# Kernel tuning notes

Hardware: AMD Instinct MI355X
Metric: run time of the kernel (lower is better)

The kernel has to match this reference:

```python
import jax, jax.numpy as jnp
import numpy as np

EPS = 1e-6
TEMP_GEO = 0.07
W_LOCAL = 0.5
W_SHARP = 0.5


def _l2norm(x):
    return x / jnp.clip(jnp.linalg.norm(x, axis=-1, keepdims=True), 1e-12)


def setup_inputs() -> dict:
    key = jax.random.key(0)
    ks = jax.random.split(key, 6)
    B, L, S, C = 8, 1024, 1024, 128
    N, P = 8, 256
    q_geo = _l2norm(jax.random.normal(ks[0], (B, L, C), jnp.float32))
    geo_pos = _l2norm(jax.random.normal(ks[1], (B, S, C), jnp.float32))
    label = jax.random.randint(ks[2], (B, L, S), 0, 2, jnp.int32)
    q_cl = jax.random.normal(ks[3], (N, P, C), jnp.float32)
    cl_pos = jax.random.normal(ks[4], (N, P, C), jnp.float32)
    idx = jax.random.randint(ks[5], (N,), 0, P, jnp.int32)
    return {"q_geo": q_geo, "q_cl": q_cl, "geo_pos": geo_pos,
            "cl_pos": cl_pos, "label": label, "idx": idx}


def _masked_mean(v, m):
    # per-sample mean over the [L,S] plane of entries where m is True
    m = m.astype(v.dtype)
    return jnp.sum(v * m, axis=(1, 2)) / jnp.maximum(jnp.sum(m, axis=(1, 2)), 1.0)


def _loftr_loss(conf, label):
    # standard LoFTR coarse CE loss (LoFTRLoss source absent from repo snippet)
    conf = jnp.clip(conf, EPS, 1.0 - EPS)
    pos = label == 1
    neg = label == 0
    pos_loss = _masked_mean(-jnp.log(conf), pos)          # [B]
    neg_loss = _masked_mean(-jnp.log(1.0 - conf), neg)    # [B]
    loss = pos_loss + neg_loss
    return jnp.mean(loss), jnp.mean(pos_loss), jnp.mean(neg_loss)


def _geometric_loss(q, k, label):
    sim = jnp.einsum('blc,bsc->bls', q, k) / TEMP_GEO        # [B,L,S]
    conf = jax.nn.softmax(sim, axis=1) * jax.nn.softmax(sim, axis=2)
    return _loftr_loss(conf, label)


def _sharpness_loss(q, k, label):
    sim = (1.0 + jnp.einsum('blc,bsc->bls', q, k)) / 2.0     # [B,L,S]
    # column stats (over L, dim=0 per sample) -> sharpness1 [B,S]
    s1 = (jnp.max(sim, axis=1) - jnp.mean(sim, axis=1)) / jnp.std(sim, axis=1, ddof=1)
    sharp1 = jax.nn.softmax(s1, axis=-1)
    # row stats (over S, dim=1 per sample) -> sharpness2 [B,L]
    s2 = (jnp.max(sim, axis=2) - jnp.mean(sim, axis=2)) / jnp.std(sim, axis=2, ddof=1)
    sharp2 = jax.nn.softmax(s2, axis=-1)
    simc = jnp.clip(sim, EPS, 1.0 - EPS)
    nll = -jnp.log(simc)
    pos = (label == 1).astype(simc.dtype)
    neg = (label == 0)
    loss1 = jnp.sum(nll * sharp1[:, None, :] * pos, axis=(1, 2))   # [B]
    loss2 = jnp.sum(nll * sharp2[:, :, None] * pos, axis=(1, 2))   # [B]
    loss3 = _masked_mean(-jnp.log(1.0 - simc), neg)                # [B]
    losses = (loss1 + loss2) / 2.0 + loss3
    return sharp1, jnp.mean(losses)


def _contrast_loss(q, all_k):
    # intended math of GeCoContrast: full cosine matrix, diag positives, tail negatives
    N = q.shape[0]
    sim = (1.0 + _l2norm(q) @ _l2norm(all_k).T) / 2.0   # [N, M]
    sim = jnp.clip(sim, EPS, 1.0 - EPS)
    l_pos = jnp.diagonal(sim[:, :N])                    # [N]
    l_neg = sim[:, N:]                                  # [N, M-N]
    return (jnp.mean(-jnp.log(l_pos)) + jnp.mean(-jnp.log(1.0 - l_neg))) / 2.0


def _forward(q_geo, q_cl, geo_pos, cl_pos, label, idx):
    loss_geo, geo_pos_loss, geo_neg_loss = _geometric_loss(q_geo, geo_pos, label)
    sharpness, loss_sharp = _sharpness_loss(q_geo, geo_pos, label)
    loss_geo = ((1.0 - W_SHARP) * loss_geo + W_SHARP * loss_sharp) * W_LOCAL

    N, P, C = q_cl.shape
    ar = jnp.arange(N)
    q_sel = q_cl[ar, idx]                               # [N,C]
    sel = cl_pos[ar, idx]                               # [N,C] positives moved to slot 0
    first = cl_pos[:, 0, :]
    swapped = cl_pos.at[ar, idx].set(first).at[:, 0, :].set(sel)
    cl_pos_save = sel
    all_k = jnp.concatenate([swapped[:, 0, :],
                             swapped[:, 1:, :].reshape(N * (P - 1), C)], axis=0)
    loss_cl = _contrast_loss(q_sel, all_k) * (1.0 - W_LOCAL)

    total = loss_geo + loss_cl
    return (sharpness, cl_pos_save, total, geo_pos_loss, geo_neg_loss, loss_sharp, loss_cl)


def reference(q_geo, q_cl, geo_pos, cl_pos, label, idx):
    return _forward(q_geo, q_cl, geo_pos, cl_pos, label, idx)
```

## Files before the change

kernel.cpp:

```cpp
#include <hip/hip_runtime.h>
#include <math.h>

#define BB 8
#define LL 1024
#define SS 1024
#define CC 128
#define NN 8
#define PP 256

static constexpr float EPS       = 1e-6f;
static constexpr float ONE_M_EPS = 1.0f - 1e-6f;
static constexpr float INV_T     = 1.0f / 0.07f;
static constexpr float NLL_MAX   = 13.815511f;
static constexpr float NLL_MIN   = 1.0000005e-6f;

static constexpr size_t DOTSZ      = (size_t)BB * LL * SS;
static constexpr size_t OFF_LSER   = DOTSZ;
static constexpr size_t OFF_LSEC   = DOTSZ + 16384;
static constexpr size_t OFF_SHARP2 = DOTSZ + 32768;
static constexpr size_t OFF_RP     = DOTSZ + 40960;
static constexpr size_t OFF_CP     = OFF_RP + 524288;
static constexpr size_t OFF_ACC    = OFF_CP + 524288;
static constexpr size_t OFF_ACCCL  = OFF_ACC + 48;
static constexpr size_t OFF_QN     = OFF_ACC + 64;

static constexpr int OUT_CLSAVE = 8192;
static constexpr int OUT_SCAL   = 9216;

typedef __bf16 bf16x8 __attribute__((ext_vector_type(8)));
typedef float  floatx4 __attribute__((ext_vector_type(4)));

__device__ __forceinline__ bf16x8 mkfrag(unsigned a, unsigned b, unsigned c, unsigned d) {
    uint4 t = make_uint4(a, b, c, d);
    return __builtin_bit_cast(bf16x8, t);
}

__device__ __forceinline__ void split_f4(float4 x,
                                         unsigned& hp0, unsigned& hp1,
                                         unsigned& lp0, unsigned& lp1) {
    unsigned u0 = __builtin_bit_cast(unsigned, x.x);
    unsigned u1 = __builtin_bit_cast(unsigned, x.y);
    unsigned u2 = __builtin_bit_cast(unsigned, x.z);
    unsigned u3 = __builtin_bit_cast(unsigned, x.w);
    unsigned r0 = u0 + 0x7FFFu + ((u0 >> 16) & 1u);
    unsigned r1 = u1 + 0x7FFFu + ((u1 >> 16) & 1u);
    unsigned r2 = u2 + 0x7FFFu + ((u2 >> 16) & 1u);
    unsigned r3 = u3 + 0x7FFFu + ((u3 >> 16) & 1u);
    float s0 = x.x - __builtin_bit_cast(float, r0 & 0xFFFF0000u);
    float s1 = x.y - __builtin_bit_cast(float, r1 & 0xFFFF0000u);
    float s2 = x.z - __builtin_bit_cast(float, r2 & 0xFFFF0000u);
    float s3 = x.w - __builtin_bit_cast(float, r3 & 0xFFFF0000u);
    hp0 = __builtin_amdgcn_perm(r1, r0, 0x07060302u);
    hp1 = __builtin_amdgcn_perm(r3, r2, 0x07060302u);
    lp0 = __builtin_amdgcn_perm(__builtin_bit_cast(unsigned, s1),
                                __builtin_bit_cast(unsigned, s0), 0x07060302u);
    lp1 = __builtin_amdgcn_perm(__builtin_bit_cast(unsigned, s3),
                                __builtin_bit_cast(unsigned, s2), 0x07060302u);
}

__device__ __forceinline__ void frag_from_lds(const float* tile, int row, int q,
                                              bf16x8& hi, bf16x8& lo) {
    const float* rp = tile + row * 32;
    int sw = row & 7;
    float4 x0 = *(const float4*)(rp + (((q * 2)     ^ sw) * 4));
    float4 x1 = *(const float4*)(rp + (((q * 2 + 1) ^ sw) * 4));
    unsigned h0, h1, h2, h3, l0, l1, l2, l3;
    split_f4(x0, h0, h1, l0, l1);
    split_f4(x1, h2, h3, l2, l3);
    hi = mkfrag(h0, h1, h2, h3);
    lo = mkfrag(l0, l1, l2, l3);
}

__global__ __launch_bounds__(256, 2) void gemm_dot(const float* __restrict__ A,
                                                   const float* __restrict__ Bm,
                                                   const float* __restrict__ q_cl,
                                                   const float* __restrict__ cl_pos,
                                                   const int* __restrict__ idx,
                                                   float* __restrict__ out,
                                                   float* __restrict__ dot,
                                                   float* __restrict__ ws) {
    __shared__ __align__(16) float ldsA[2][128 * 32];
    __shared__ __align__(16) float ldsB[2][128 * 32];

    int tid  = threadIdx.x;
    int lane = tid & 63;
    int w    = tid >> 6;

    if (blockIdx.x == 512) {
        if (tid < 52) ws[OFF_ACC + tid] = 0.0f;
        for (int n = w; n < NN; n += 4) {
            int in = idx[n];
            const float* q = q_cl + ((size_t)(n * PP + in)) * CC;
            float2 qv = *(const float2*)(q + 2 * lane);
            float ss = qv.x * qv.x + qv.y * qv.y;
            for (int o = 32; o; o >>= 1) ss += __shfl_xor(ss, o);
            float inv = 1.0f / fmaxf(sqrtf(ss), 1e-12f);
            *(float2*)(ws + OFF_QN + n * 128 + 2 * lane) = make_float2(qv.x * inv, qv.y * inv);
            const float* cp = cl_pos + ((size_t)(n * PP + in)) * CC;
            float2 cv = *(const float2*)(cp + 2 * lane);
            *(float2*)(out + OUT_CLSAVE + n * 128 + 2 * lane) = cv;
        }
        return;
    }

    int t  = blockIdx.x;
    int b  = t >> 6;
    int rm = t & 63;
    int bl = rm >> 3, bs = rm & 7;
    int R0 = bl * 128, C0 = bs * 128;

    const float* Ab = A  + ((size_t)b * LL + R0) * CC;
    const float* Bb = Bm + ((size_t)b * SS + C0) * CC;

    const float* src  = (w >= 2) ? Bb : Ab;
    float* dst0 = (w >= 2) ? ldsB[0] : ldsA[0];
    float* dst1 = (w >= 2) ? ldsB[1] : ldsA[1];
    int L       = ((w & 1) << 6) | lane;
    int rowoff  = L >> 3;
    int chunk   = L & 7;
    int swz4    = (chunk ^ (rowoff & 7)) * 4;

    int fl   = lane & 15;
    int quad = lane >> 4;
    int wr   = w >> 1, wc = w & 1;
    int Rw   = wr * 64, Cw = wc * 64;

    floatx4 acc[4][4];
#pragma unroll
    for (int i = 0; i < 4; i++)
#pragma unroll
        for (int j = 0; j < 4; j++) acc[i][j] = (floatx4){0.f, 0.f, 0.f, 0.f};

    float4 rg[8];
#pragma unroll
    for (int i = 0; i < 8; i++)
        rg[i] = *(const float4*)(src + (size_t)(i * 16 + rowoff) * CC + chunk * 4);
#pragma unroll
    for (int i = 0; i < 8; i++)
        *(float4*)(dst0 + (i * 16 + rowoff) * 32 + swz4) = rg[i];
    __syncthreads();

    for (int ks = 0; ks < 4; ks++) {
        const float* la = (ks & 1) ? ldsA[1] : ldsA[0];
        const float* lb = (ks & 1) ? ldsB[1] : ldsB[0];
        float* nxt = ((ks + 1) & 1) ? dst1 : dst0;
        if (ks < 3) {
            int k0 = (ks + 1) * 32;
#pragma unroll
            for (int i = 0; i < 8; i++)
                rg[i] = *(const float4*)(src + (size_t)(i * 16 + rowoff) * CC + k0 + chunk * 4);
        }
        bf16x8 ah[4], al[4];
#pragma unroll
        for (int mt = 0; mt < 4; mt++)
            frag_from_lds(la, Rw + mt * 16 + fl, quad, ah[mt], al[mt]);
#pragma unroll
        for (int nt = 0; nt < 4; nt++) {
            bf16x8 bh, blo;
            frag_from_lds(lb, Cw + nt * 16 + fl, quad, bh, blo);
#pragma unroll
            for (int mt = 0; mt < 4; mt++) {
                acc[mt][nt] = __builtin_amdgcn_mfma_f32_16x16x32_bf16(ah[mt], bh,  acc[mt][nt], 0, 0, 0);
                acc[mt][nt] = __builtin_amdgcn_mfma_f32_16x16x32_bf16(ah[mt], blo, acc[mt][nt], 0, 0, 0);
                acc[mt][nt] = __builtin_amdgcn_mfma_f32_16x16x32_bf16(al[mt], bh,  acc[mt][nt], 0, 0, 0);
            }
        }
        if (ks < 3) {
#pragma unroll
            for (int i = 0; i < 8; i++)
                *(float4*)(nxt + (i * 16 + rowoff) * 32 + swz4) = rg[i];
        }
        __syncthreads();
    }

#pragma unroll
    for (int mt = 0; mt < 4; mt++)
#pragma unroll
        for (int nt = 0; nt < 4; nt++) {
            int col = C0 + Cw + nt * 16 + fl;
#pragma unroll
            for (int r = 0; r < 4; r++) {
                int row = R0 + Rw + mt * 16 + quad * 4 + r;
                dot[((size_t)(b * 1024 + row)) * 1024 + col] = acc[mt][nt][r];
            }
        }

    int stile = bs * 2 + wc;
    int ltile = bl * 2 + wr;
    float ces[4], cmx[4], csm[4], csq[4];
#pragma unroll
    for (int nt = 0; nt < 4; nt++) { ces[nt] = 0.f; cmx[nt] = -1e30f; csm[nt] = 0.f; csq[nt] = 0.f; }
#pragma unroll
    for (int mt = 0; mt < 4; mt++) {
#pragma unroll
        for (int r = 0; r < 4; r++) {
            float es = 0.f, mx = -1e30f, sm = 0.f, sq = 0.f;
#pragma unroll
            for (int nt = 0; nt < 4; nt++) {
                float d  = acc[mt][nt][r];
                float e  = __expf(d * INV_T);
                float s2 = fmaf(0.5f, d, 0.5f);
                es += e; mx = fmaxf(mx, s2); sm += s2; sq += s2 * s2;
                ces[nt] += e; cmx[nt] = fmaxf(cmx[nt], s2); csm[nt] += s2; csq[nt] += s2 * s2;
            }
            for (int o = 1; o < 16; o <<= 1) {
                es += __shfl_xor(es, o);
                mx = fmaxf(mx, __shfl_xor(mx, o));
                sm += __shfl_xor(sm, o);
                sq += __shfl_xor(sq, o);
            }
            if (fl == 0) {
                int row = R0 + Rw + mt * 16 + quad * 4 + r;
                *(float4*)(ws + OFF_RP + (((size_t)(b * 16 + stile)) * 1024 + row) * 4) =
                    make_float4(es, mx, sm, sq);
            }
        }
    }
#pragma unroll
    for (int nt = 0; nt < 4; nt++) {
        float es = ces[nt], mx = cmx[nt], sm = csm[nt], sq = csq[nt];
        for (int o = 16; o < 64; o <<= 1) {
            es += __shfl_xor(es, o);
            mx = fmaxf(mx, __shfl_xor(mx, o));
            sm += __shfl_xor(sm, o);
            sq += __shfl_xor(sq, o);
        }
        if (quad == 0) {
            int col = C0 + Cw + nt * 16 + fl;
            *(float4*)(ws + OFF_CP + (((size_t)(b * 16 + ltile)) * 1024 + col) * 4) =
                make_float4(es, mx, sm, sq);
        }
    }
}

__global__ __launch_bounds__(256) void mid(const float* __restrict__ cl_pos,
                                           const int* __restrict__ idx,
                                           float* __restrict__ ws,
                                           float* __restrict__ out) {
    int q   = blockIdx.x;
    int tid = threadIdx.x;
    int lane = tid & 63, wid = tid >> 6;

    if (q < 16) {
        bool docol = (q < 8);
        int b = q & 7;
        const float* part = ws + (docol ? OFF_CP : OFF_RP);
        float* lse = ws + (docol ? OFF_LSEC : OFF_LSER) + (size_t)b * 1024;
        float zs[4];
        float mxall = -1e30f;
#pragma unroll
        for (int r = 0; r < 4; r++) {
            int i = tid + r * 256;
            float es = 0.f, mx = -1e30f, sm = 0.f, sq = 0.f;
#pragma unroll
            for (int t = 0; t < 16; t++) {
                float4 v = *(const float4*)(part + (((size_t)(b * 16 + t)) * 1024 + i) * 4);
                es += v.x; mx = fmaxf(mx, v.y); sm += v.z; sq += v.w;
            }
            float mean = sm * (1.0f / 1024.0f);
            float var  = (sq - sm * sm * (1.0f / 1024.0f)) * (1.0f / 1023.0f);
            zs[r] = (mx - mean) / sqrtf(fmaxf(var, 1e-30f));
            mxall = fmaxf(mxall, zs[r]);
            lse[i] = __logf(es);
        }
        __shared__ float sb[4];
        __shared__ float red;
        float mx = mxall;
        for (int o = 32; o; o >>= 1) mx = fmaxf(mx, __shfl_xor(mx, o));
        if (!lane) sb[wid] = mx;
        __syncthreads();
        if (tid == 0) red = fmaxf(fmaxf(sb[0], sb[1]), fmaxf(sb[2], sb[3]));
        __syncthreads();
        mx = red;
        float e[4]; float smv = 0.f;
#pragma unroll
        for (int r = 0; r < 4; r++) { e[r] = __expf(zs[r] - mx); smv += e[r]; }
        for (int o = 32; o; o >>= 1) smv += __shfl_xor(smv, o);
        __syncthreads();
        if (!lane) sb[wid] = smv;
        __syncthreads();
        if (tid == 0) red = sb[0] + sb[1] + sb[2] + sb[3];
        __syncthreads();
        float inv = 1.0f / red;
        float* dst = docol ? (out + (size_t)b * 1024) : (ws + OFF_SHARP2 + (size_t)b * 1024);
#pragma unroll
        for (int r = 0; r < 4; r++) dst[tid + r * 256] = e[r] * inv;
    } else {
        int j = (q - 16) * 4 + wid;
        int m, p;
        if (j < NN) {
            m = j; p = idx[j];
        } else {
            int jj = j - NN;
            m = jj / (PP - 1);
            p = 1 + (jj - m * (PP - 1));
            if (p == idx[m]) p = 0;
        }
        const float* k = cl_pos + ((size_t)(m * PP + p)) * CC;
        float2 kv = *(const float2*)(k + 2 * lane);
        float ksq = kv.x * kv.x + kv.y * kv.y;
        for (int o = 32; o; o >>= 1) ksq += __shfl_xor(ksq, o);
        float invkn = 1.0f / fmaxf(sqrtf(ksq), 1e-12f);
        float pos = 0.0f, neg = 0.0f;
        if (j < NN) {
            const float2 qv = *(const float2*)(ws + OFF_QN + j * 128 + 2 * lane);
            float dt = qv.x * kv.x + qv.y * kv.y;
            for (int o = 32; o; o >>= 1) dt += __shfl_xor(dt, o);
            float sim = fminf(fmaxf(fmaf(0.5f * invkn, dt, 0.5f), EPS), ONE_M_EPS);
            pos = -__logf(sim);
        } else {
#pragma unroll
            for (int n = 0; n < NN; n++) {
                const float2 qv = *(const float2*)(ws + OFF_QN + n * 128 + 2 * lane);
                float dt = qv.x * kv.x + qv.y * kv.y;
                for (int o = 32; o; o >>= 1) dt += __shfl_xor(dt, o);
                float om = fminf(fmaxf(fmaf(-0.5f * invkn, dt, 0.5f), EPS), ONE_M_EPS);
                neg -= __logf(om);
            }
        }
        __shared__ float cb[2][4];
        if (!lane) { cb[0][wid] = pos; cb[1][wid] = neg; }
        __syncthreads();
        if (tid == 0) {
            float ps = cb[0][0] + cb[0][1] + cb[0][2] + cb[0][3];
            float ng = cb[1][0] + cb[1][1] + cb[1][2] + cb[1][3];
            if (ps != 0.0f) atomicAdd(ws + OFF_ACCCL + 0, ps);
            if (ng != 0.0f) atomicAdd(ws + OFF_ACCCL + 1, ng);
        }
    }
}

__device__ __forceinline__ void proc_elem(float d, int lab, float lcj, float sh1j,
                                          float lr, float s2v,
                                          float& posg, float& negg, float& l1, float& l2,
                                          float& negs, float& pcf) {
    float t = lr + lcj - d * (2.0f * INV_T);
    float isPos = (lab == 1) ? 1.0f : 0.0f;
    float isNeg = 1.0f - isPos;
    float tp   = fminf(fmaxf(t, NLL_MIN), NLL_MAX);
    float simc = fminf(fmaxf(fmaf(0.5f, d, 0.5f), EPS), ONE_M_EPS);
    float om   = fminf(fmaxf(fmaf(-0.5f, d, 0.5f), EPS), ONE_M_EPS);
    float nll2 = -__logf(simc);
    float cf   = fminf(fmaxf(__expf(-t), EPS), ONE_M_EPS);
    float nllg = -__logf(1.0f - cf);
    float nlls = -__logf(om);
    posg += isPos * tp;
    l1   += isPos * nll2 * sh1j;
    l2   += isPos * nll2 * s2v;
    pcf  += isPos;
    negg += isNeg * nllg;
    negs += isNeg * nlls;
}

__global__ __launch_bounds__(256) void main_loss(const float* __restrict__ dot,
                                                 const int* __restrict__ label,
                                                 const float* __restrict__ sharp1,
                                                 float* __restrict__ ws) {
    int b = blockIdx.y;
    int l0 = blockIdx.x * 4;
    int s = threadIdx.x * 4;
    float4 lc4 = *(const float4*)(ws + OFF_LSEC + (size_t)b * 1024 + s);
    float4 sh1 = *(const float4*)(sharp1 + (size_t)b * 1024 + s);
    const float* lser = ws + OFF_LSER + (size_t)b * 1024;
    const float* sh2  = ws + OFF_SHARP2 + (size_t)b * 1024;
    float posg = 0, negg = 0, l1 = 0, l2 = 0, negs = 0, pcf = 0;
#pragma unroll
    for (int r = 0; r < 4; r++) {
        int l = l0 + r;
        float lr  = lser[l];
        float s2v = sh2[l];
        size_t base = ((size_t)(b * 1024 + l)) * 1024 + s;
        float4 d4 = *(const float4*)(dot + base);
        int4  lb  = *(const int4*)(label + base);
        proc_elem(d4.x, lb.x, lc4.x, sh1.x, lr, s2v, posg, negg, l1, l2, negs, pcf);
        proc_elem(d4.y, lb.y, lc4.y, sh1.y, lr, s2v, posg, negg, l1, l2, negs, pcf);
        proc_elem(d4.z, lb.z, lc4.z, sh1.z, lr, s2v, posg, negg, l1, l2, negs, pcf);
        proc_elem(d4.w, lb.w, lc4.w, sh1.w, lr, s2v, posg, negg, l1, l2, negs, pcf);
    }
    float vals[6] = {posg, negg, l1, l2, negs, pcf};
    __shared__ float sb[6][4];
    int lane = threadIdx.x & 63, wid = threadIdx.x >> 6;
#pragma unroll
    for (int k = 0; k < 6; k++) {
        float v = vals[k];
        for (int o = 32; o; o >>= 1) v += __shfl_xor(v, o);
        if (!lane) sb[k][wid] = v;
    }
    __syncthreads();
    if (threadIdx.x < 6) {
        float r = sb[threadIdx.x][0] + sb[threadIdx.x][1] + sb[threadIdx.x][2] + sb[threadIdx.x][3];
        atomicAdd(ws + OFF_ACC + (size_t)b * 6 + threadIdx.x, r);
    }
}

__global__ void finalize(float* __restrict__ out, const float* __restrict__ ws) {
    if (threadIdx.x != 0) return;
    float gp = 0, gn = 0, lsh = 0;
    for (int b = 0; b < 8; b++) {
        const float* a = ws + OFF_ACC + (size_t)b * 6;
        float pc = a[5];
        float nc = (float)((size_t)LL * SS) - pc;
        gp += a[0] / fmaxf(pc, 1.0f);
        gn += a[1] / fmaxf(nc, 1.0f);
        lsh += (a[2] + a[3]) * 0.5f + a[4] / fmaxf(nc, 1.0f);
    }
    gp *= 0.125f; gn *= 0.125f; lsh *= 0.125f;
    float lgeo = gp + gn;
    float lgw = (0.5f * lgeo + 0.5f * lsh) * 0.5f;
    float clp = ws[OFF_ACCCL + 0] / 8.0f;
    float cln = ws[OFF_ACCCL + 1] / (8.0f * 2040.0f);
    float lcl = (clp + cln) * 0.5f * 0.5f;
    out[OUT_SCAL + 0] = lgw + lcl;
    out[OUT_SCAL + 1] = gp;
    out[OUT_SCAL + 2] = gn;
    out[OUT_SCAL + 3] = lsh;
    out[OUT_SCAL + 4] = lcl;
}

extern "C" void kernel_launch(void* const* d_in, const int* in_sizes, int n_in,
                              void* d_out, int out_size, void* d_ws, size_t ws_size,
                              hipStream_t stream) {
    const float* q_geo   = (const float*)d_in[0];
    const float* q_cl    = (const float*)d_in[1];
    const float* geo_pos = (const float*)d_in[2];
    const float* cl_pos  = (const float*)d_in[3];
    const int*   label   = (const int*)d_in[4];
    const int*   idx     = (const int*)d_in[5];
    float* out = (float*)d_out;
    float* ws  = (float*)d_ws;
    float* dot = ws;

    gemm_dot<<<dim3(513), dim3(256), 0, stream>>>(q_geo, geo_pos, q_cl, cl_pos, idx, out, dot, ws);
    mid<<<dim3(528), dim3(256), 0, stream>>>(cl_pos, idx, ws, out);
    main_loss<<<dim3(256, 8), dim3(256), 0, stream>>>(dot, label, out, ws);
    finalize<<<dim3(1), dim3(64), 0, stream>>>(out, ws);
}
```

Before: 148.3 us.

## Presplit fp32 inputs into bf16 hi/lo pairs in a separate kernel before GEMM

Adds a presplit kernel that converts q_geo and geo_pos once into packed bf16 hi/lo halves stored in workspace. The GEMM then loads these prepacked fragments straight from LDS instead of re-splitting fp32 values per tile. This removes redundant split arithmetic, since each input row was previously split by 8 blocks. The cost is an extra kernel launch plus an extra round trip through global memory for the split data.

```diff
diff --git a/kernel.cpp b/kernel.cpp
--- a/kernel.cpp
+++ b/kernel.cpp
@@ -23,17 +23,14 @@
 static constexpr size_t OFF_ACC    = OFF_CP + 524288;
 static constexpr size_t OFF_ACCCL  = OFF_ACC + 48;
 static constexpr size_t OFF_QN     = OFF_ACC + 64;
+static constexpr size_t OFF_ASP    = OFF_ACC + 2048;
+static constexpr size_t OFF_BSP    = OFF_ASP + 1048576;
 
 static constexpr int OUT_CLSAVE = 8192;
 static constexpr int OUT_SCAL   = 9216;
 
 typedef __bf16 bf16x8 __attribute__((ext_vector_type(8)));
 typedef float  floatx4 __attribute__((ext_vector_type(4)));
-
-__device__ __forceinline__ bf16x8 mkfrag(unsigned a, unsigned b, unsigned c, unsigned d) {
-    uint4 t = make_uint4(a, b, c, d);
-    return __builtin_bit_cast(bf16x8, t);
-}
 
 __device__ __forceinline__ void split_f4(float4 x,
                                          unsigned& hp0, unsigned& hp1,
@@ -58,35 +55,16 @@
                                 __builtin_bit_cast(unsigned, s2), 0x07060302u);
 }
 
-__device__ __forceinline__ void frag_from_lds(const float* tile, int row, int q,
-                                              bf16x8& hi, bf16x8& lo) {
-    const float* rp = tile + row * 32;
-    int sw = row & 7;
-    float4 x0 = *(const float4*)(rp + (((q * 2)     ^ sw) * 4));
-    float4 x1 = *(const float4*)(rp + (((q * 2 + 1) ^ sw) * 4));
-    unsigned h0, h1, h2, h3, l0, l1, l2, l3;
-    split_f4(x0, h0, h1, l0, l1);
-    split_f4(x1, h2, h3, l2, l3);
-    hi = mkfrag(h0, h1, h2, h3);
-    lo = mkfrag(l0, l1, l2, l3);
-}
-
-__global__ __launch_bounds__(256, 2) void gemm_dot(const float* __restrict__ A,
-                                                   const float* __restrict__ Bm,
-                                                   const float* __restrict__ q_cl,
-                                                   const float* __restrict__ cl_pos,
-                                                   const int* __restrict__ idx,
-                                                   float* __restrict__ out,
-                                                   float* __restrict__ dot,
-                                                   float* __restrict__ ws) {
-    __shared__ __align__(16) float ldsA[2][128 * 32];
-    __shared__ __align__(16) float ldsB[2][128 * 32];
-
-    int tid  = threadIdx.x;
-    int lane = tid & 63;
-    int w    = tid >> 6;
-
-    if (blockIdx.x == 512) {
+__global__ __launch_bounds__(256) void presplit(const float* __restrict__ A,
+                                                const float* __restrict__ Bm,
+                                                const float* __restrict__ q_cl,
+                                                const float* __restrict__ cl_pos,
+                                                const int* __restrict__ idx,
+                                                float* __restrict__ out,
+                                                float* __restrict__ ws) {
+    int tid = threadIdx.x;
+    if (blockIdx.x == 1024) {
+        int lane = tid & 63, w = tid >> 6;
         if (tid < 52) ws[OFF_ACC + tid] = 0.0f;
         for (int n = w; n < NN; n += 4) {
             int in = idx[n];
@@ -102,6 +80,28 @@
         }
         return;
     }
+    int bb  = blockIdx.x;
+    int mat = bb >> 9;
+    size_t grow = (size_t)(bb & 511) * 16 + (tid >> 4);
+    int c   = tid & 15;
+    const float* in = (mat ? Bm : A) + grow * CC + c * 8;
+    float4 v0 = *(const float4*)in;
+    float4 v1 = *(const float4*)(in + 4);
+    unsigned h0, h1, l0, l1, h2, h3, l2, l3;
+    split_f4(v0, h0, h1, l0, l1);
+    split_f4(v1, h2, h3, l2, l3);
+    float* outp = ws + (mat ? OFF_BSP : OFF_ASP) + grow * 128 + (size_t)(c >> 2) * 32 + (c & 3) * 4;
+    *(uint4*)outp        = make_uint4(h0, h1, h2, h3);
+    *(uint4*)(outp + 16) = make_uint4(l0, l1, l2, l3);
+}
+
+__global__ __launch_bounds__(256, 2) void gemm_dot(float* __restrict__ dot,
+                                                   float* __restrict__ ws) {
+    __shared__ __align__(16) char lds[2][32768];
+
+    int tid  = threadIdx.x;
+    int lane = tid & 63;
+    int w    = tid >> 6;
 
     int t  = blockIdx.x;
     int b  = t >> 6;
@@ -109,16 +109,21 @@
     int bl = rm >> 3, bs = rm & 7;
     int R0 = bl * 128, C0 = bs * 128;
 
-    const float* Ab = A  + ((size_t)b * LL + R0) * CC;
-    const float* Bb = Bm + ((size_t)b * SS + C0) * CC;
-
-    const float* src  = (w >= 2) ? Bb : Ab;
-    float* dst0 = (w >= 2) ? ldsB[0] : ldsA[0];
-    float* dst1 = (w >= 2) ? ldsB[1] : ldsA[1];
-    int L       = ((w & 1) << 6) | lane;
-    int rowoff  = L >> 3;
-    int chunk   = L & 7;
-    int swz4    = (chunk ^ (rowoff & 7)) * 4;
+    const float* Ab = ws + OFF_ASP + ((size_t)(b * 1024 + R0)) * 128;
+    const float* Bb = ws + OFF_BSP + ((size_t)(b * 1024 + C0)) * 128;
+
+    const float* srcp[8];
+    int ldsb[8];
+#pragma unroll
+    for (int i = 0; i < 8; i++) {
+        int g   = i * 256 + tid;
+        int mat = g >> 10;
+        int r   = (g >> 3) & 127;
+        int pc  = g & 7;
+        int c   = pc ^ (r & 7);
+        srcp[i] = (mat ? Bb : Ab) + (size_t)r * 128 + (c >> 2) * 16 + (c & 3) * 4;
+        ldsb[i] = g * 16;
+    }
 
     int fl   = lane & 15;
     int quad = lane >> 4;
@@ -131,33 +136,36 @@
 #pragma unroll
         for (int j = 0; j < 4; j++) acc[i][j] = (floatx4){0.f, 0.f, 0.f, 0.f};
 
-    float4 rg[8];
-#pragma unroll
-    for (int i = 0; i < 8; i++)
-        rg[i] = *(const float4*)(src + (size_t)(i * 16 + rowoff) * CC + chunk * 4);
-#pragma unroll
-    for (int i = 0; i < 8; i++)
-        *(float4*)(dst0 + (i * 16 + rowoff) * 32 + swz4) = rg[i];
+    uint4 rg[8];
+#pragma unroll
+    for (int i = 0; i < 8; i++) rg[i] = *(const uint4*)(srcp[i]);
+#pragma unroll
+    for (int i = 0; i < 8; i++) *(uint4*)(&lds[0][ldsb[i]]) = rg[i];
     __syncthreads();
 
     for (int ks = 0; ks < 4; ks++) {
-        const float* la = (ks & 1) ? ldsA[1] : ldsA[0];
-        const float* lb = (ks & 1) ? ldsB[1] : ldsB[0];
-        float* nxt = ((ks + 1) & 1) ? dst1 : dst0;
+        int cur = ks & 1;
         if (ks < 3) {
-            int k0 = (ks + 1) * 32;
 #pragma unroll
             for (int i = 0; i < 8; i++)
-                rg[i] = *(const float4*)(src + (size_t)(i * 16 + rowoff) * CC + k0 + chunk * 4);
-        }
+                rg[i] = *(const uint4*)(srcp[i] + (ks + 1) * 32);
+        }
+        const char* la = lds[cur];
+        const char* lb = lds[cur] + 16384;
         bf16x8 ah[4], al[4];
 #pragma unroll
-        for (int mt = 0; mt < 4; mt++)
-            frag_from_lds(la, Rw + mt * 16 + fl, quad, ah[mt], al[mt]);
+        for (int mt = 0; mt < 4; mt++) {
+            int row = Rw + mt * 16 + fl;
+            int sw  = row & 7;
+            ah[mt] = *(const bf16x8*)(la + row * 128 + ((quad ^ sw) * 16));
+            al[mt] = *(const bf16x8*)(la + row * 128 + (((quad + 4) ^ sw) * 16));
+        }
 #pragma unroll
         for (int nt = 0; nt < 4; nt++) {
-            bf16x8 bh, blo;
-            frag_from_lds(lb, Cw + nt * 16 + fl, quad, bh, blo);
+            int row = Cw + nt * 16 + fl;
+            int sw  = row & 7;
+            bf16x8 bh  = *(const bf16x8*)(lb + row * 128 + ((quad ^ sw) * 16));
+            bf16x8 blo = *(const bf16x8*)(lb + row * 128 + (((quad + 4) ^ sw) * 16));
 #pragma unroll
             for (int mt = 0; mt < 4; mt++) {
                 acc[mt][nt] = __builtin_amdgcn_mfma_f32_16x16x32_bf16(ah[mt], bh,  acc[mt][nt], 0, 0, 0);
@@ -166,9 +174,9 @@
             }
         }
         if (ks < 3) {
-#pragma unroll
-            for (int i = 0; i < 8; i++)
-                *(float4*)(nxt + (i * 16 + rowoff) * 32 + swz4) = rg[i];
+            char* nxt = lds[cur ^ 1];
+#pragma unroll
+            for (int i = 0; i < 8; i++) *(uint4*)(&nxt[ldsb[i]]) = rg[i];
         }
         __syncthreads();
     }
@@ -430,7 +438,8 @@
     float* ws  = (float*)d_ws;
     float* dot = ws;
 
-    gemm_dot<<<dim3(513), dim3(256), 0, stream>>>(q_geo, geo_pos, q_cl, cl_pos, idx, out, dot, ws);
+    presplit<<<dim3(1025), dim3(256), 0, stream>>>(q_geo, geo_pos, q_cl, cl_pos, idx, out, ws);
+    gemm_dot<<<dim3(512), dim3(256), 0, stream>>>(dot, ws);
     mid<<<dim3(528), dim3(256), 0, stream>>>(cl_pos, idx, ws, out);
     main_loss<<<dim3(256, 8), dim3(256), 0, stream>>>(dot, label, out, ws);
     finalize<<<dim3(1), dim3(64), 0, stream>>>(out, ws);
```

After: 151.9 us. 2.4% more time.
